# Kernel optimization log

Hardware: AMD Instinct MI355X
Metric: run time of the kernel (lower is better)

The kernel has to match this reference:

```python
import jax, jax.numpy as jnp
import numpy as np

D_MODEL = 1024
N_HEAD = 16
D_K = D_MODEL // N_HEAD


def setup_inputs() -> dict:
    key = jax.random.key(0)
    k1, k2, k3 = jax.random.split(key, 3)
    B, S = 2, 2048
    x = jax.random.normal(k1, (B, S, D_MODEL), dtype=jnp.float32)
    attention_mask = jnp.ones((B, 1, 1, S), dtype=jnp.float32)
    # Conv1D params: weight [nx, nf], bias [nf]; init std=0.02 per source
    W_attn = 0.02 * jax.random.normal(k2, (D_MODEL, 3 * D_MODEL), dtype=jnp.float32)
    b_attn = jnp.zeros((3 * D_MODEL,), dtype=jnp.float32)
    W_proj = 0.02 * jax.random.normal(k3, (D_MODEL, D_MODEL), dtype=jnp.float32)
    b_proj = jnp.zeros((D_MODEL,), dtype=jnp.float32)
    return {"x": x, "attention_mask": attention_mask,
            "W_attn": W_attn, "b_attn": b_attn,
            "W_proj": W_proj, "b_proj": b_proj}


def reference(x, attention_mask, W_attn, b_attn, W_proj, b_proj):
    B, S, _ = x.shape
    # c_attn: fused QKV projection (Conv1D == addmm)
    qkv = x @ W_attn + b_attn                       # [B, S, 3*D]
    q, k, v = jnp.split(qkv, 3, axis=-1)            # each [B, S, D]

    def split_heads(t):                             # [B, S, D] -> [B, H, S, d_k]
        return t.reshape(B, S, N_HEAD, D_K).transpose(0, 2, 1, 3)

    q, k, v = split_heads(q), split_heads(k), split_heads(v)
    scale = 1.0 / jnp.sqrt(jnp.float32(D_K))
    scores = jnp.einsum("bhqd,bhkd->bhqk", q, k) * scale   # [B, H, S, S]
    scores = scores + (1.0 - attention_mask) * -10000.0
    scores = jax.nn.softmax(scores, axis=-1)
    # dropout omitted (eval / deterministic)
    out = jnp.einsum("bhqk,bhkd->bhqd", scores, v)          # [B, H, S, d_k]
    out = out.transpose(0, 2, 1, 3).reshape(B, S, D_MODEL)  # merge heads
    out = out @ W_proj + b_proj                             # c_proj
    return out, scores
```

## Files before the change

### kernel.cpp

```cpp
#include <hip/hip_runtime.h>

typedef unsigned short u16;
typedef __bf16 bf16x8 __attribute__((ext_vector_type(8)));
typedef float f32x4 __attribute__((ext_vector_type(4)));

#define D_MODEL 1024
#define S_LEN 2048
#define NH 16
#define DK 64
#define BATCH 2
#define M_ROWS (BATCH * S_LEN)
#define NQKV (3 * D_MODEL)

__device__ __forceinline__ u16 f2bf(float x) {
  union { __bf16 h; u16 u; } v; v.h = (__bf16)x;
  return v.u;
}
__device__ __forceinline__ float bf2f(u16 b) {
  union { unsigned u; float f; } v; v.u = ((unsigned)b) << 16; return v.f;
}
__device__ __forceinline__ void gload16(const void* g, void* l) {
  __builtin_amdgcn_global_load_lds((const __attribute__((address_space(1))) unsigned int*)g,
                                   (__attribute__((address_space(3))) unsigned int*)l, 16, 0, 0);
}

__global__ __launch_bounds__(256) void pack_bf16(const float* __restrict__ in, u16* __restrict__ out) {
  const int idx = (blockIdx.x * 256 + threadIdx.x) * 8;
  float4 a = *(const float4*)&in[idx];
  float4 b = *(const float4*)&in[idx + 4];
  unsigned p0 = (unsigned)f2bf(a.x) | ((unsigned)f2bf(a.y) << 16);
  unsigned p1 = (unsigned)f2bf(a.z) | ((unsigned)f2bf(a.w) << 16);
  unsigned p2 = (unsigned)f2bf(b.x) | ((unsigned)f2bf(b.y) << 16);
  unsigned p3 = (unsigned)f2bf(b.z) | ((unsigned)f2bf(b.w) << 16);
  int4 o; o.x = (int)p0; o.y = (int)p1; o.z = (int)p2; o.w = (int)p3;
  *(int4*)&out[idx] = o;
}

__global__ __launch_bounds__(256) void transpose_pack(const float* __restrict__ in, u16* __restrict__ out,
                                                      int R, int C) {
  __shared__ u16 T[64][68];
  const int r0 = blockIdx.x * 64, c0 = blockIdx.y * 64;
  const int t = threadIdx.x;
  const int col = t & 63, rq = t >> 6;
#pragma unroll
  for (int s = 0; s < 16; ++s) {
    int row = s * 4 + rq;
    T[col][row] = f2bf(in[(size_t)(r0 + row) * C + c0 + col]);
  }
  __syncthreads();
#pragma unroll
  for (int s = 0; s < 16; ++s) {
    int crow = s * 4 + rq;
    out[(size_t)(c0 + crow) * R + r0 + col] = T[crow][col];
  }
}

template <int OUTF32>
__global__ __launch_bounds__(256) void gemm_bt(const u16* __restrict__ A, const u16* __restrict__ BT,
                                               const float* __restrict__ bias, void* __restrict__ outp,
                                               int K, int N) {
  __shared__ u16 As[2][128 * 64];
  __shared__ u16 Bs[2][128 * 64];
  const int m0 = blockIdx.x * 128, n0 = blockIdx.y * 128;
  const int t = threadIdx.x, lane = t & 63, w = t >> 6;
  const int wr = w >> 1, wc = w & 1;
  const int l15 = lane & 15, l4 = lane >> 4;
  const int srow = lane >> 3, schunk = lane & 7;

  f32x4 acc[4][4] = {};

#define STAGE_G(buf, k0)                                                        \
  do {                                                                          \
    _Pragma("unroll") for (int i = 0; i < 4; ++i) {                             \
      int r0 = (i * 4 + w) * 8;                                                 \
      int r = r0 + srow;                                                        \
      int sc = (schunk ^ (r & 7)) * 8;                                          \
      gload16(&A[(size_t)(m0 + r) * K + (k0) + sc], &As[buf][r0 * 64]);         \
      gload16(&BT[(size_t)(n0 + r) * K + (k0) + sc], &Bs[buf][r0 * 64]);        \
    }                                                                           \
  } while (0)

  STAGE_G(0, 0);
  __syncthreads();
  const int nk = K / 64;
  int cur = 0;
  for (int t0 = 0; t0 < nk; ++t0) {
    if (t0 + 1 < nk) STAGE_G(cur ^ 1, (t0 + 1) * 64);
#pragma unroll
    for (int ks = 0; ks < 2; ++ks) {
      bf16x8 af[4], bfr[4];
#pragma unroll
      for (int g = 0; g < 4; ++g) {
        int ra = wr * 64 + g * 16 + l15;
        int rb = wc * 64 + g * 16 + l15;
        af[g]  = *(const bf16x8*)&As[cur][ra * 64 + ((ks * 4 + l4) ^ (ra & 7)) * 8];
        bfr[g] = *(const bf16x8*)&Bs[cur][rb * 64 + ((ks * 4 + l4) ^ (rb & 7)) * 8];
      }
#pragma unroll
      for (int mg = 0; mg < 4; ++mg)
#pragma unroll
        for (int ng = 0; ng < 4; ++ng)
          acc[mg][ng] = __builtin_amdgcn_mfma_f32_16x16x32_bf16(af[mg], bfr[ng], acc[mg][ng], 0, 0, 0);
    }
    __syncthreads();
    cur ^= 1;
  }
#undef STAGE_G
  const int rowb = m0 + wr * 64, colb = n0 + wc * 64;
#pragma unroll
  for (int mg = 0; mg < 4; ++mg)
#pragma unroll
    for (int ng = 0; ng < 4; ++ng) {
      int col = colb + ng * 16 + l15;
      float bv = bias[col];
#pragma unroll
      for (int j = 0; j < 4; ++j) {
        int row = rowb + mg * 16 + l4 * 4 + j;
        float val = acc[mg][ng][j] + bv;
        if (OUTF32) ((float*)outp)[(size_t)row * N + col] = val;
        else        ((u16*)outp)[(size_t)row * N + col] = f2bf(val);
      }
    }
}

__global__ __launch_bounds__(512, 4) void attn_fused(const u16* __restrict__ qkv, const float* __restrict__ mask,
                                                     float* __restrict__ scores, u16* __restrict__ attnout) {
  __shared__ u16 Ks[2][64 * 64];
  __shared__ u16 Vt[2][64 * 68];
  __shared__ u16 Ps[8][16][72];
  __shared__ float MB[S_LEN];
  const int bid = blockIdx.x;
  const int qt = bid & 15, h = (bid >> 4) & 15, b = bid >> 8;
  const int t = threadIdx.x, lane = t & 63, w = t >> 6;
  const int l15 = lane & 15, l4 = lane >> 4;
  const u16* kbase = qkv + (size_t)b * S_LEN * NQKV + D_MODEL + h * DK;
  const u16* vbase = kbase + D_MODEL;

  {
    float4 m4 = *(const float4*)&mask[b * S_LEN + t * 4];
    MB[t * 4 + 0] = -10000.0f * (1.0f - m4.x);
    MB[t * 4 + 1] = -10000.0f * (1.0f - m4.y);
    MB[t * 4 + 2] = -10000.0f * (1.0f - m4.z);
    MB[t * 4 + 3] = -10000.0f * (1.0f - m4.w);
  }

  bf16x8 qf[2];
  {
    const int qrow = qt * 128 + w * 16 + l15;
    const u16* qp = qkv + (size_t)(b * S_LEN + qrow) * NQKV + h * DK;
#pragma unroll
    for (int ks = 0; ks < 2; ++ks) {
      union { bf16x8 v; u16 s[8]; } qa;
      qa.v = *(const bf16x8*)&qp[ks * 32 + l4 * 8];
#pragma unroll
      for (int e = 0; e < 8; ++e) qa.s[e] = f2bf(bf2f(qa.s[e]) * 0.125f);
      qf[ks] = qa.v;
    }
  }

  const int krow = w * 8 + (lane >> 3);
  const int kchunk = ((lane & 7) ^ (krow & 7)) * 8;
#define STAGE_K(buf, kt) \
  gload16(&kbase[(size_t)((kt) * 64 + krow) * NQKV + kchunk], &Ks[buf][w * 512])

  float ps4[4] = {0.f, 0.f, 0.f, 0.f};
  int cur = 0;
  STAGE_K(0, 0);
  __syncthreads();
  for (int kt = 0; kt < 32; ++kt) {
    if (kt + 1 < 32) STAGE_K(cur ^ 1, kt + 1);
    f32x4 sacc[4] = {};
#pragma unroll
    for (int ks = 0; ks < 2; ++ks) {
      bf16x8 kf[4];
#pragma unroll
      for (int n = 0; n < 4; ++n) {
        int kr = n * 16 + l15;
        kf[n] = *(const bf16x8*)&Ks[cur][kr * 64 + ((ks * 4 + l4) ^ (kr & 7)) * 8];
      }
#pragma unroll
      for (int n = 0; n < 4; ++n)
        sacc[n] = __builtin_amdgcn_mfma_f32_16x16x32_bf16(qf[ks], kf[n], sacc[n], 0, 0, 0);
    }
#pragma unroll
    for (int n = 0; n < 4; ++n) {
      float mb = MB[kt * 64 + n * 16 + l15];
#pragma unroll
      for (int j = 0; j < 4; ++j) ps4[j] += __expf(sacc[n][j] + mb);
    }
    __syncthreads();
    cur ^= 1;
  }
#pragma unroll
  for (int off = 1; off < 16; off <<= 1)
#pragma unroll
    for (int j = 0; j < 4; ++j) ps4[j] += __shfl_xor(ps4[j], off, 64);
  float inv4[4];
#pragma unroll
  for (int j = 0; j < 4; ++j) inv4[j] = 1.0f / ps4[j];

  f32x4 oacc[4] = {};
  const int vr = t >> 3, vc = (t & 7) * 8;
  const size_t sbase = ((size_t)((b * NH + h) * S_LEN + qt * 128 + w * 16 + l4 * 4)) * S_LEN + l15;

  STAGE_K(0, 0);
  {
    const u16* vp = &vbase[(size_t)vr * NQKV + vc];
    int4 va0 = *(const int4*)vp;
    const u16* s0 = (const u16*)&va0;
#pragma unroll
    for (int i = 0; i < 8; ++i) Vt[0][(vc + i) * 68 + vr] = s0[i];
  }
  __syncthreads();
  cur = 0;
  for (int kt = 0; kt < 32; ++kt) {
    const bool hn = (kt + 1 < 32);
    int4 va;
    if (hn) {
      STAGE_K(cur ^ 1, kt + 1);
      va = *(const int4*)&vbase[(size_t)((kt + 1) * 64 + vr) * NQKV + vc];
    }
    f32x4 sacc[4] = {};
#pragma unroll
    for (int ks = 0; ks < 2; ++ks) {
      bf16x8 kf[4];
#pragma unroll
      for (int n = 0; n < 4; ++n) {
        int kr = n * 16 + l15;
        kf[n] = *(const bf16x8*)&Ks[cur][kr * 64 + ((ks * 4 + l4) ^ (kr & 7)) * 8];
      }
#pragma unroll
      for (int n = 0; n < 4; ++n)
        sacc[n] = __builtin_amdgcn_mfma_f32_16x16x32_bf16(qf[ks], kf[n], sacc[n], 0, 0, 0);
    }
#pragma unroll
    for (int n = 0; n < 4; ++n) {
      float mb = MB[kt * 64 + n * 16 + l15];
#pragma unroll
      for (int j = 0; j < 4; ++j) {
        float p = __expf(sacc[n][j] + mb) * inv4[j];
        scores[sbase + (size_t)j * S_LEN + kt * 64 + n * 16] = p;
        Ps[w][l4 * 4 + j][n * 16 + l15] = f2bf(p);
      }
    }
#pragma unroll
    for (int ks = 0; ks < 2; ++ks) {
      bf16x8 pa = *(const bf16x8*)&Ps[w][l15][ks * 32 + l4 * 8];
      bf16x8 vf[4];
#pragma unroll
      for (int dn = 0; dn < 4; ++dn)
        vf[dn] = *(const bf16x8*)&Vt[cur][(dn * 16 + l15) * 68 + ks * 32 + l4 * 8];
#pragma unroll
      for (int dn = 0; dn < 4; ++dn)
        oacc[dn] = __builtin_amdgcn_mfma_f32_16x16x32_bf16(pa, vf[dn], oacc[dn], 0, 0, 0);
    }
    if (hn) {
      const u16* s0 = (const u16*)&va;
#pragma unroll
      for (int i = 0; i < 8; ++i) Vt[cur ^ 1][(vc + i) * 68 + vr] = s0[i];
    }
    __syncthreads();
    cur ^= 1;
  }
#undef STAGE_K
#pragma unroll
  for (int dn = 0; dn < 4; ++dn) {
    int row = b * S_LEN + qt * 128 + w * 16 + l4 * 4;
    int col = h * DK + dn * 16 + l15;
#pragma unroll
    for (int j = 0; j < 4; ++j)
      attnout[(size_t)(row + j) * D_MODEL + col] = f2bf(oacc[dn][j]);
  }
}

extern "C" void kernel_launch(void* const* d_in, const int* in_sizes, int n_in,
                              void* d_out, int out_size, void* d_ws, size_t ws_size,
                              hipStream_t stream) {
  const float* x      = (const float*)d_in[0];
  const float* mask   = (const float*)d_in[1];
  const float* W_attn = (const float*)d_in[2];
  const float* b_attn = (const float*)d_in[3];
  const float* W_proj = (const float*)d_in[4];
  const float* b_proj = (const float*)d_in[5];
  float* out    = (float*)d_out;
  float* scores = out + (size_t)M_ROWS * D_MODEL;

  char* ws = (char*)d_ws;
  u16* xb     = (u16*)ws;
  u16* wqkvT  = (u16*)(ws + (size_t)(8  << 20));
  u16* wprojT = (u16*)(ws + (size_t)(14 << 20));
  u16* qkv    = (u16*)(ws + (size_t)(16 << 20));
  u16* attnb  = (u16*)(ws + (size_t)(40 << 20));

  pack_bf16<<<(M_ROWS * D_MODEL) / (256 * 8), 256, 0, stream>>>(x, xb);
  transpose_pack<<<dim3(D_MODEL / 64, NQKV / 64), 256, 0, stream>>>(W_attn, wqkvT, D_MODEL, NQKV);
  transpose_pack<<<dim3(D_MODEL / 64, D_MODEL / 64), 256, 0, stream>>>(W_proj, wprojT, D_MODEL, D_MODEL);
  gemm_bt<0><<<dim3(M_ROWS / 128, NQKV / 128), 256, 0, stream>>>(xb, wqkvT, b_attn, (void*)qkv, D_MODEL, NQKV);
  attn_fused<<<BATCH * NH * (S_LEN / 128), 512, 0, stream>>>(qkv, mask, scores, attnb);
  gemm_bt<1><<<dim3(M_ROWS / 128, D_MODEL / 128), 256, 0, stream>>>(attnb, wprojT, b_proj, (void*)out, D_MODEL, D_MODEL);
}
```

Measured before the change: 233.5 us.

## Split softmax row-sum pass into separate register-tiled kernel

The first pass of the attention kernel, which recomputes QK^T to get the softmax denominators, moves into its own kernel. In that kernel each wave computes a 64x32 tile, so every K fragment loaded from LDS is reused across four query groups. The attention kernel then reads the precomputed inverse row sums from workspace. The block index is also remapped so that blocks launched together share batch-head groups, which should improve L2 locality. The cost is an extra kernel launch and a small global round trip for the row sums.

```diff
diff --git a/kernel.cpp b/kernel.cpp
--- a/kernel.cpp
+++ b/kernel.cpp
@@ -123,14 +123,119 @@
     }
 }
 
+__global__ __launch_bounds__(256, 4) void qk_rowsum(const u16* __restrict__ qkv, const float* __restrict__ mask,
+                                                    float* __restrict__ rowinv) {
+  __shared__ u16 Ks[2][64 * 64];
+  __shared__ float MB[S_LEN];
+  __shared__ float RS[128][2];
+  const int bid = blockIdx.x;
+  const int low = bid & 7, rest = bid >> 3;
+  const int qt = rest & 15;
+  const int bh = (rest >> 4) * 8 + low;
+  const int b = bh >> 4, h = bh & 15;
+  const int t = threadIdx.x, lane = t & 63, w = t >> 6;
+  const int wr = w >> 1, wc = w & 1;
+  const int l15 = lane & 15, l4 = lane >> 4;
+  const u16* kbase = qkv + (size_t)b * S_LEN * NQKV + D_MODEL + h * DK;
+
+  {
+    float4 m0 = *(const float4*)&mask[b * S_LEN + t * 8];
+    float4 m1 = *(const float4*)&mask[b * S_LEN + t * 8 + 4];
+    MB[t * 8 + 0] = -10000.0f * (1.0f - m0.x); MB[t * 8 + 1] = -10000.0f * (1.0f - m0.y);
+    MB[t * 8 + 2] = -10000.0f * (1.0f - m0.z); MB[t * 8 + 3] = -10000.0f * (1.0f - m0.w);
+    MB[t * 8 + 4] = -10000.0f * (1.0f - m1.x); MB[t * 8 + 5] = -10000.0f * (1.0f - m1.y);
+    MB[t * 8 + 6] = -10000.0f * (1.0f - m1.z); MB[t * 8 + 7] = -10000.0f * (1.0f - m1.w);
+  }
+
+  bf16x8 qf[4][2];
+#pragma unroll
+  for (int mg = 0; mg < 4; ++mg) {
+    int qrow = qt * 128 + wr * 64 + mg * 16 + l15;
+    const u16* qp = qkv + (size_t)(b * S_LEN + qrow) * NQKV + h * DK;
+#pragma unroll
+    for (int ks = 0; ks < 2; ++ks) {
+      union { bf16x8 v; u16 s[8]; } qa;
+      qa.v = *(const bf16x8*)&qp[ks * 32 + l4 * 8];
+#pragma unroll
+      for (int e = 0; e < 8; ++e) qa.s[e] = f2bf(bf2f(qa.s[e]) * 0.125f);
+      qf[mg][ks] = qa.v;
+    }
+  }
+
+  const int krow8 = lane >> 3, kch = lane & 7;
+#define STAGE_KA(buf, kt)                                                             \
+  do {                                                                                \
+    _Pragma("unroll") for (int i = 0; i < 2; ++i) {                                   \
+      int r = i * 32 + w * 8 + krow8;                                                 \
+      int sc = (kch ^ (r & 7)) * 8;                                                   \
+      gload16(&kbase[(size_t)((kt) * 64 + r) * NQKV + sc], &Ks[buf][i * 2048 + w * 512]); \
+    }                                                                                 \
+  } while (0)
+
+  float rs[4][4] = {};
+  STAGE_KA(0, 0);
+  __syncthreads();
+  int cur = 0;
+  for (int kt = 0; kt < 32; ++kt) {
+    if (kt + 1 < 32) STAGE_KA(cur ^ 1, kt + 1);
+    f32x4 sacc[4][2] = {};
+#pragma unroll
+    for (int ks = 0; ks < 2; ++ks) {
+      bf16x8 kf[2];
+#pragma unroll
+      for (int nn = 0; nn < 2; ++nn) {
+        int kr = (wc * 2 + nn) * 16 + l15;
+        kf[nn] = *(const bf16x8*)&Ks[cur][kr * 64 + ((ks * 4 + l4) ^ (kr & 7)) * 8];
+      }
+#pragma unroll
+      for (int mg = 0; mg < 4; ++mg)
+#pragma unroll
+        for (int nn = 0; nn < 2; ++nn)
+          sacc[mg][nn] = __builtin_amdgcn_mfma_f32_16x16x32_bf16(qf[mg][ks], kf[nn], sacc[mg][nn], 0, 0, 0);
+    }
+#pragma unroll
+    for (int nn = 0; nn < 2; ++nn) {
+      float mb = MB[kt * 64 + (wc * 2 + nn) * 16 + l15];
+#pragma unroll
+      for (int mg = 0; mg < 4; ++mg)
+#pragma unroll
+        for (int j = 0; j < 4; ++j)
+          rs[mg][j] += __expf(sacc[mg][nn][j] + mb);
+    }
+    __syncthreads();
+    cur ^= 1;
+  }
+#undef STAGE_KA
+#pragma unroll
+  for (int off = 1; off < 16; off <<= 1)
+#pragma unroll
+    for (int mg = 0; mg < 4; ++mg)
+#pragma unroll
+      for (int j = 0; j < 4; ++j)
+        rs[mg][j] += __shfl_xor(rs[mg][j], off, 64);
+  if (l15 == 0)
+#pragma unroll
+    for (int mg = 0; mg < 4; ++mg)
+#pragma unroll
+      for (int j = 0; j < 4; ++j)
+        RS[wr * 64 + mg * 16 + l4 * 4 + j][wc] = rs[mg][j];
+  __syncthreads();
+  if (t < 128)
+    rowinv[(size_t)(b * NH + h) * S_LEN + qt * 128 + t] = 1.0f / (RS[t][0] + RS[t][1]);
+}
+
 __global__ __launch_bounds__(512, 4) void attn_fused(const u16* __restrict__ qkv, const float* __restrict__ mask,
+                                                     const float* __restrict__ rowinv,
                                                      float* __restrict__ scores, u16* __restrict__ attnout) {
   __shared__ u16 Ks[2][64 * 64];
   __shared__ u16 Vt[2][64 * 68];
   __shared__ u16 Ps[8][16][72];
   __shared__ float MB[S_LEN];
   const int bid = blockIdx.x;
-  const int qt = bid & 15, h = (bid >> 4) & 15, b = bid >> 8;
+  const int low = bid & 7, rest = bid >> 3;
+  const int qt = rest & 15;
+  const int bh = (rest >> 4) * 8 + low;
+  const int b = bh >> 4, h = bh & 15;
   const int t = threadIdx.x, lane = t & 63, w = t >> 6;
   const int l15 = lane & 15, l4 = lane >> 4;
   const u16* kbase = qkv + (size_t)b * S_LEN * NQKV + D_MODEL + h * DK;
@@ -158,46 +263,15 @@
     }
   }
 
+  float inv4[4];
+#pragma unroll
+  for (int j = 0; j < 4; ++j)
+    inv4[j] = rowinv[(size_t)(b * NH + h) * S_LEN + qt * 128 + w * 16 + l4 * 4 + j];
+
   const int krow = w * 8 + (lane >> 3);
   const int kchunk = ((lane & 7) ^ (krow & 7)) * 8;
 #define STAGE_K(buf, kt) \
   gload16(&kbase[(size_t)((kt) * 64 + krow) * NQKV + kchunk], &Ks[buf][w * 512])
-
-  float ps4[4] = {0.f, 0.f, 0.f, 0.f};
-  int cur = 0;
-  STAGE_K(0, 0);
-  __syncthreads();
-  for (int kt = 0; kt < 32; ++kt) {
-    if (kt + 1 < 32) STAGE_K(cur ^ 1, kt + 1);
-    f32x4 sacc[4] = {};
-#pragma unroll
-    for (int ks = 0; ks < 2; ++ks) {
-      bf16x8 kf[4];
-#pragma unroll
-      for (int n = 0; n < 4; ++n) {
-        int kr = n * 16 + l15;
-        kf[n] = *(const bf16x8*)&Ks[cur][kr * 64 + ((ks * 4 + l4) ^ (kr & 7)) * 8];
-      }
-#pragma unroll
-      for (int n = 0; n < 4; ++n)
-        sacc[n] = __builtin_amdgcn_mfma_f32_16x16x32_bf16(qf[ks], kf[n], sacc[n], 0, 0, 0);
-    }
-#pragma unroll
-    for (int n = 0; n < 4; ++n) {
-      float mb = MB[kt * 64 + n * 16 + l15];
-#pragma unroll
-      for (int j = 0; j < 4; ++j) ps4[j] += __expf(sacc[n][j] + mb);
-    }
-    __syncthreads();
-    cur ^= 1;
-  }
-#pragma unroll
-  for (int off = 1; off < 16; off <<= 1)
-#pragma unroll
-    for (int j = 0; j < 4; ++j) ps4[j] += __shfl_xor(ps4[j], off, 64);
-  float inv4[4];
-#pragma unroll
-  for (int j = 0; j < 4; ++j) inv4[j] = 1.0f / ps4[j];
 
   f32x4 oacc[4] = {};
   const int vr = t >> 3, vc = (t & 7) * 8;
@@ -212,7 +286,7 @@
     for (int i = 0; i < 8; ++i) Vt[0][(vc + i) * 68 + vr] = s0[i];
   }
   __syncthreads();
-  cur = 0;
+  int cur = 0;
   for (int kt = 0; kt < 32; ++kt) {
     const bool hn = (kt + 1 < 32);
     int4 va;
@@ -286,16 +360,18 @@
   float* scores = out + (size_t)M_ROWS * D_MODEL;
 
   char* ws = (char*)d_ws;
-  u16* xb     = (u16*)ws;
-  u16* wqkvT  = (u16*)(ws + (size_t)(8  << 20));
-  u16* wprojT = (u16*)(ws + (size_t)(14 << 20));
-  u16* qkv    = (u16*)(ws + (size_t)(16 << 20));
-  u16* attnb  = (u16*)(ws + (size_t)(40 << 20));
+  u16* xb      = (u16*)ws;
+  u16* wqkvT   = (u16*)(ws + (size_t)(8  << 20));
+  u16* wprojT  = (u16*)(ws + (size_t)(14 << 20));
+  u16* qkv     = (u16*)(ws + (size_t)(16 << 20));
+  u16* attnb   = (u16*)(ws + (size_t)(40 << 20));
+  float* rowinv = (float*)(ws + (size_t)(48 << 20));
 
   pack_bf16<<<(M_ROWS * D_MODEL) / (256 * 8), 256, 0, stream>>>(x, xb);
   transpose_pack<<<dim3(D_MODEL / 64, NQKV / 64), 256, 0, stream>>>(W_attn, wqkvT, D_MODEL, NQKV);
   transpose_pack<<<dim3(D_MODEL / 64, D_MODEL / 64), 256, 0, stream>>>(W_proj, wprojT, D_MODEL, D_MODEL);
   gemm_bt<0><<<dim3(M_ROWS / 128, NQKV / 128), 256, 0, stream>>>(xb, wqkvT, b_attn, (void*)qkv, D_MODEL, NQKV);
-  attn_fused<<<BATCH * NH * (S_LEN / 128), 512, 0, stream>>>(qkv, mask, scores, attnb);
+  qk_rowsum<<<BATCH * NH * (S_LEN / 128), 256, 0, stream>>>(qkv, mask, rowinv);
+  attn_fused<<<BATCH * NH * (S_LEN / 128), 512, 0, stream>>>(qkv, mask, rowinv, scores, attnb);
   gemm_bt<1><<<dim3(M_ROWS / 128, D_MODEL / 128), 256, 0, stream>>>(attnb, wprojT, b_proj, (void*)out, D_MODEL, D_MODEL);
 }
```

After: 261.1 us. 1.12x slower.

## Split attention key tiles across warp pairs with 64-row query blocks

Applied to the files above, without the earlier changes.

The attention kernel now processes 64 query rows per block instead of 128. The 8 warps form 4 query groups by 2 key halves, so each warp handles half of every 64-key tile. Row sums and partial PV outputs are combined through shared memory, and the mask is read directly from global memory instead of a shared-memory bias table. Doubling the grid and shrinking LDS use is meant to raise occupancy and parallelism. The cost is twice the K/V tile loads and recomputed QK^T across blocks, plus extra reductions and syncs.

```diff
diff --git a/kernel.cpp b/kernel.cpp
--- a/kernel.cpp
+++ b/kernel.cpp
@@ -123,30 +123,24 @@
     }
 }
 
-__global__ __launch_bounds__(512, 4) void attn_fused(const u16* __restrict__ qkv, const float* __restrict__ mask,
+__global__ __launch_bounds__(512, 6) void attn_fused(const u16* __restrict__ qkv, const float* __restrict__ mask,
                                                      float* __restrict__ scores, u16* __restrict__ attnout) {
   __shared__ u16 Ks[2][64 * 64];
   __shared__ u16 Vt[2][64 * 68];
-  __shared__ u16 Ps[8][16][72];
-  __shared__ float MB[S_LEN];
+  __shared__ u16 Ps[8][16][40];
+  __shared__ float RS[4][16][2];
   const int bid = blockIdx.x;
-  const int qt = bid & 15, h = (bid >> 4) & 15, b = bid >> 8;
+  const int qt = bid & 31, h = (bid >> 5) & 15, b = bid >> 9;
   const int t = threadIdx.x, lane = t & 63, w = t >> 6;
+  const int qg = w >> 1, kg = w & 1;
   const int l15 = lane & 15, l4 = lane >> 4;
   const u16* kbase = qkv + (size_t)b * S_LEN * NQKV + D_MODEL + h * DK;
   const u16* vbase = kbase + D_MODEL;
-
-  {
-    float4 m4 = *(const float4*)&mask[b * S_LEN + t * 4];
-    MB[t * 4 + 0] = -10000.0f * (1.0f - m4.x);
-    MB[t * 4 + 1] = -10000.0f * (1.0f - m4.y);
-    MB[t * 4 + 2] = -10000.0f * (1.0f - m4.z);
-    MB[t * 4 + 3] = -10000.0f * (1.0f - m4.w);
-  }
+  const float* mrow = mask + b * S_LEN;
 
   bf16x8 qf[2];
   {
-    const int qrow = qt * 128 + w * 16 + l15;
+    const int qrow = qt * 64 + qg * 16 + l15;
     const u16* qp = qkv + (size_t)(b * S_LEN + qrow) * NQKV + h * DK;
 #pragma unroll
     for (int ks = 0; ks < 2; ++ks) {
@@ -158,8 +152,8 @@
     }
   }
 
-  const int krow = w * 8 + (lane >> 3);
-  const int kchunk = ((lane & 7) ^ (krow & 7)) * 8;
+  const int krow = t >> 3;
+  const int kchunk = ((t & 7) ^ (krow & 7)) * 8;
 #define STAGE_K(buf, kt) \
   gload16(&kbase[(size_t)((kt) * 64 + krow) * NQKV + kchunk], &Ks[buf][w * 512])
 
@@ -169,22 +163,23 @@
   __syncthreads();
   for (int kt = 0; kt < 32; ++kt) {
     if (kt + 1 < 32) STAGE_K(cur ^ 1, kt + 1);
-    f32x4 sacc[4] = {};
+    f32x4 sacc[2] = {};
 #pragma unroll
     for (int ks = 0; ks < 2; ++ks) {
-      bf16x8 kf[4];
-#pragma unroll
-      for (int n = 0; n < 4; ++n) {
-        int kr = n * 16 + l15;
+      bf16x8 kf[2];
+#pragma unroll
+      for (int n = 0; n < 2; ++n) {
+        int kr = kg * 32 + n * 16 + l15;
         kf[n] = *(const bf16x8*)&Ks[cur][kr * 64 + ((ks * 4 + l4) ^ (kr & 7)) * 8];
       }
 #pragma unroll
-      for (int n = 0; n < 4; ++n)
+      for (int n = 0; n < 2; ++n)
         sacc[n] = __builtin_amdgcn_mfma_f32_16x16x32_bf16(qf[ks], kf[n], sacc[n], 0, 0, 0);
     }
 #pragma unroll
-    for (int n = 0; n < 4; ++n) {
-      float mb = MB[kt * 64 + n * 16 + l15];
+    for (int n = 0; n < 2; ++n) {
+      float m = mrow[kt * 64 + kg * 32 + n * 16 + l15];
+      float mb = -10000.0f * (1.0f - m);
 #pragma unroll
       for (int j = 0; j < 4; ++j) ps4[j] += __expf(sacc[n][j] + mb);
     }
@@ -195,13 +190,17 @@
   for (int off = 1; off < 16; off <<= 1)
 #pragma unroll
     for (int j = 0; j < 4; ++j) ps4[j] += __shfl_xor(ps4[j], off, 64);
+  if (l15 == 0)
+#pragma unroll
+    for (int j = 0; j < 4; ++j) RS[qg][l4 * 4 + j][kg] = ps4[j];
+  __syncthreads();
   float inv4[4];
 #pragma unroll
-  for (int j = 0; j < 4; ++j) inv4[j] = 1.0f / ps4[j];
+  for (int j = 0; j < 4; ++j) inv4[j] = 1.0f / (RS[qg][l4 * 4 + j][0] + RS[qg][l4 * 4 + j][1]);
 
   f32x4 oacc[4] = {};
   const int vr = t >> 3, vc = (t & 7) * 8;
-  const size_t sbase = ((size_t)((b * NH + h) * S_LEN + qt * 128 + w * 16 + l4 * 4)) * S_LEN + l15;
+  const size_t sbase = ((size_t)((b * NH + h) * S_LEN + qt * 64 + qg * 16 + l4 * 4)) * S_LEN + l15;
 
   STAGE_K(0, 0);
   {
@@ -220,36 +219,36 @@
       STAGE_K(cur ^ 1, kt + 1);
       va = *(const int4*)&vbase[(size_t)((kt + 1) * 64 + vr) * NQKV + vc];
     }
-    f32x4 sacc[4] = {};
+    f32x4 sacc[2] = {};
 #pragma unroll
     for (int ks = 0; ks < 2; ++ks) {
-      bf16x8 kf[4];
-#pragma unroll
-      for (int n = 0; n < 4; ++n) {
-        int kr = n * 16 + l15;
+      bf16x8 kf[2];
+#pragma unroll
+      for (int n = 0; n < 2; ++n) {
+        int kr = kg * 32 + n * 16 + l15;
         kf[n] = *(const bf16x8*)&Ks[cur][kr * 64 + ((ks * 4 + l4) ^ (kr & 7)) * 8];
       }
 #pragma unroll
-      for (int n = 0; n < 4; ++n)
+      for (int n = 0; n < 2; ++n)
         sacc[n] = __builtin_amdgcn_mfma_f32_16x16x32_bf16(qf[ks], kf[n], sacc[n], 0, 0, 0);
     }
 #pragma unroll
-    for (int n = 0; n < 4; ++n) {
-      float mb = MB[kt * 64 + n * 16 + l15];
+    for (int n = 0; n < 2; ++n) {
+      float m = mrow[kt * 64 + kg * 32 + n * 16 + l15];
+      float mb = -10000.0f * (1.0f - m);
 #pragma unroll
       for (int j = 0; j < 4; ++j) {
         float p = __expf(sacc[n][j] + mb) * inv4[j];
-        scores[sbase + (size_t)j * S_LEN + kt * 64 + n * 16] = p;
+        scores[sbase + (size_t)j * S_LEN + kt * 64 + kg * 32 + n * 16] = p;
         Ps[w][l4 * 4 + j][n * 16 + l15] = f2bf(p);
       }
     }
-#pragma unroll
-    for (int ks = 0; ks < 2; ++ks) {
-      bf16x8 pa = *(const bf16x8*)&Ps[w][l15][ks * 32 + l4 * 8];
+    {
+      bf16x8 pa = *(const bf16x8*)&Ps[w][l15][l4 * 8];
       bf16x8 vf[4];
 #pragma unroll
       for (int dn = 0; dn < 4; ++dn)
-        vf[dn] = *(const bf16x8*)&Vt[cur][(dn * 16 + l15) * 68 + ks * 32 + l4 * 8];
+        vf[dn] = *(const bf16x8*)&Vt[cur][(dn * 16 + l15) * 68 + kg * 32 + l4 * 8];
 #pragma unroll
       for (int dn = 0; dn < 4; ++dn)
         oacc[dn] = __builtin_amdgcn_mfma_f32_16x16x32_bf16(pa, vf[dn], oacc[dn], 0, 0, 0);
@@ -263,13 +262,26 @@
     cur ^= 1;
   }
 #undef STAGE_K
-#pragma unroll
-  for (int dn = 0; dn < 4; ++dn) {
-    int row = b * S_LEN + qt * 128 + w * 16 + l4 * 4;
-    int col = h * DK + dn * 16 + l15;
-#pragma unroll
-    for (int j = 0; j < 4; ++j)
-      attnout[(size_t)(row + j) * D_MODEL + col] = f2bf(oacc[dn][j]);
+  float* OX = (float*)&Ks[0][0];
+  if (kg == 1) {
+#pragma unroll
+    for (int dn = 0; dn < 4; ++dn)
+#pragma unroll
+      for (int j = 0; j < 4; ++j)
+        OX[(qg * 16 + l4 * 4 + j) * 64 + dn * 16 + l15] = oacc[dn][j];
+  }
+  __syncthreads();
+  if (kg == 0) {
+#pragma unroll
+    for (int dn = 0; dn < 4; ++dn) {
+      int col = h * DK + dn * 16 + l15;
+#pragma unroll
+      for (int j = 0; j < 4; ++j) {
+        int row = b * S_LEN + qt * 64 + qg * 16 + l4 * 4 + j;
+        float o = oacc[dn][j] + OX[(qg * 16 + l4 * 4 + j) * 64 + dn * 16 + l15];
+        attnout[(size_t)row * D_MODEL + col] = f2bf(o);
+      }
+    }
   }
 }
 
@@ -296,6 +308,6 @@
   transpose_pack<<<dim3(D_MODEL / 64, NQKV / 64), 256, 0, stream>>>(W_attn, wqkvT, D_MODEL, NQKV);
   transpose_pack<<<dim3(D_MODEL / 64, D_MODEL / 64), 256, 0, stream>>>(W_proj, wprojT, D_MODEL, D_MODEL);
   gemm_bt<0><<<dim3(M_ROWS / 128, NQKV / 128), 256, 0, stream>>>(xb, wqkvT, b_attn, (void*)qkv, D_MODEL, NQKV);
-  attn_fused<<<BATCH * NH * (S_LEN / 128), 512, 0, stream>>>(qkv, mask, scores, attnb);
+  attn_fused<<<BATCH * NH * (S_LEN / 64), 512, 0, stream>>>(qkv, mask, scores, attnb);
   gemm_bt<1><<<dim3(M_ROWS / 128, D_MODEL / 128), 256, 0, stream>>>(attnb, wprojT, b_proj, (void*)out, D_MODEL, D_MODEL);
 }
```

After: 287.4 us. 23.1% more time.
